# Performance work log

Measured on AMD Instinct MI355X. Metric: run time of the kernel, lower is better.

## Reference

```python
import jax, jax.numpy as jnp
import numpy as np
import math

DIM = 2048
N_HEADS = 16
HEAD_DIM = 128
BATCH = 2
T = 2048
EPS = 1e-5


def setup_inputs() -> dict:
    key = jax.random.key(0)
    ks = jax.random.split(key, 16)
    s = lambda fan_in: 1.0 / math.sqrt(fan_in)
    d = {}
    d['x'] = jax.random.normal(ks[0], (BATCH, T, DIM), dtype=jnp.float32)
    d['start_pos'] = 0
    # attention projections (weights stored [in, out])
    d['wq'] = jax.random.uniform(ks[1], (DIM, N_HEADS * HEAD_DIM), minval=-s(DIM), maxval=s(DIM))
    d['bq'] = jnp.zeros((N_HEADS * HEAD_DIM,), jnp.float32)
    d['wk'] = jax.random.uniform(ks[2], (DIM, HEAD_DIM), minval=-s(DIM), maxval=s(DIM))
    d['bk'] = jnp.zeros((HEAD_DIM,), jnp.float32)
    d['wv'] = jax.random.uniform(ks[3], (DIM, HEAD_DIM), minval=-s(DIM), maxval=s(DIM))
    d['bv'] = jnp.zeros((HEAD_DIM,), jnp.float32)
    d['wo'] = jax.random.uniform(ks[4], (N_HEADS * HEAD_DIM, DIM), minval=-s(N_HEADS * HEAD_DIM), maxval=s(N_HEADS * HEAD_DIM))
    d['bo'] = jnp.zeros((DIM,), jnp.float32)
    # layernorms
    d['ln1_g'] = jnp.ones((DIM,), jnp.float32)
    d['ln1_b'] = jnp.zeros((DIM,), jnp.float32)
    d['ln2_g'] = jnp.ones((DIM,), jnp.float32)
    d['ln2_b'] = jnp.zeros((DIM,), jnp.float32)
    # MLP (dim -> 4*dim -> dim), dropout p=0 is a no-op
    d['w1'] = jax.random.uniform(ks[5], (DIM, 4 * DIM), minval=-s(DIM), maxval=s(DIM))
    d['b1'] = jnp.zeros((4 * DIM,), jnp.float32)
    d['w2'] = jax.random.uniform(ks[6], (4 * DIM, DIM), minval=-s(4 * DIM), maxval=s(4 * DIM))
    d['b2'] = jnp.zeros((DIM,), jnp.float32)
    return d


def _layernorm(h, g, b):
    mu = jnp.mean(h, axis=-1, keepdims=True)
    var = jnp.mean(jnp.square(h - mu), axis=-1, keepdims=True)
    return (h - mu) * jax.lax.rsqrt(var + EPS) * g + b


def reference(x, start_pos, wq, bq, wk, bk, wv, bv, wo, bo, ln1_g, ln1_b, ln2_g, ln2_b, w1, b1, w2, b2):
    B, Tq, D = x.shape
    hd = wk.shape[1]
    H = wq.shape[1] // hd
    # --- MQA attention on pre-LN input (prefill: no kv cache) ---
    h = _layernorm(x, ln1_g, ln1_b)
    q = (h @ wq + bq).reshape(B, Tq, H, hd)          # [B,T,H,hd]
    k = h @ wk + bk                                   # [B,T,hd] single shared head
    v = h @ wv + bv                                   # [B,T,hd]
    scores = jnp.einsum('bthc,bsc->bhts', q, k) / math.sqrt(hd)
    causal = jnp.where(jnp.tril(jnp.ones((Tq, Tq), dtype=bool)), 0.0, -jnp.inf).astype(scores.dtype)
    attn = jax.nn.softmax(scores + causal, axis=-1)   # [B,H,T,T]
    ctx = jnp.einsum('bhts,bsc->bthc', attn, v).reshape(B, Tq, H * hd)
    out = ctx @ wo + bo
    x = x + out
    # --- GELU MLP (exact erf gelu, torch default) ---
    h2 = _layernorm(x, ln2_g, ln2_b)
    x = x + jax.nn.gelu(h2 @ w1 + b1, approximate=False) @ w2 + b2
    k_cat = k[:, None]                                # [B,1,T,hd]
    v_cat = v[:, None]
    return (x, k_cat, v_cat)
```

## Files before the change

### kernel.cpp

```cpp
#include <hip/hip_runtime.h>
#include <stdint.h>

#define DIMSZ 2048
#define HD 128
#define NH 16
#define BATCH 2
#define SEQ 2048
#define MROWS (BATCH*SEQ)
#define FFDIM (4*DIMSZ)
#define NQKV (DIMSZ + 2*HD)

typedef float f32x4 __attribute__((ext_vector_type(4)));
typedef __bf16 bf16x8 __attribute__((ext_vector_type(8)));
typedef __bf16 bf16_t;

__device__ __forceinline__ void async16(const void* g, void* l) {
  __builtin_amdgcn_global_load_lds(
      (const __attribute__((address_space(1))) void*)(uintptr_t)g,
      (__attribute__((address_space(3))) void*)(uint32_t)(uintptr_t)l,
      16, 0, 0);
}

__device__ __forceinline__ float gelu_f(float x) {
  return 0.5f * x * (1.0f + erff(x * 0.70710678118654752f));
}

__device__ __forceinline__ void hard_barrier() {
  asm volatile("" ::: "memory");
  __builtin_amdgcn_s_barrier();
  asm volatile("" ::: "memory");
}

__global__ __launch_bounds__(256)
void k_transpose_f32_bf16(const float* __restrict__ src, bf16_t* __restrict__ dst,
                          int R, int C) {
  __shared__ float tile[32][33];
  int c0 = blockIdx.x * 32, r0 = blockIdx.y * 32;
  int tx = threadIdx.x & 31, ty = threadIdx.x >> 5;
#pragma unroll
  for (int i = 0; i < 32; i += 8)
    tile[ty + i][tx] = src[(size_t)(r0 + ty + i) * C + (c0 + tx)];
  __syncthreads();
#pragma unroll
  for (int i = 0; i < 32; i += 8)
    dst[(size_t)(c0 + ty + i) * R + (r0 + tx)] = (bf16_t)tile[tx][ty + i];
}

__global__ __launch_bounds__(256)
void k_transpose_v(const bf16_t* __restrict__ v, bf16_t* __restrict__ vt) {
  __shared__ bf16_t tile[32][33];
  int b = blockIdx.z;
  int t0 = blockIdx.x * 32, d0 = blockIdx.y * 32;
  int tx = threadIdx.x & 31, ty = threadIdx.x >> 5;
#pragma unroll
  for (int i = 0; i < 32; i += 8)
    tile[ty + i][tx] = v[((size_t)(b * SEQ + t0 + ty + i)) * HD + d0 + tx];
  __syncthreads();
#pragma unroll
  for (int i = 0; i < 32; i += 8)
    vt[((size_t)(b * HD + d0 + ty + i)) * SEQ + t0 + tx] = tile[tx][ty + i];
}

__global__ __launch_bounds__(256)
void k_layernorm(const float* __restrict__ x, const float* __restrict__ g,
                 const float* __restrict__ bb, bf16_t* __restrict__ out) {
  int row = blockIdx.x;
  const float* xr = x + (size_t)row * DIMSZ;
  int t = threadIdx.x;
  float vals[8];
  float s = 0.f, s2 = 0.f;
#pragma unroll
  for (int i = 0; i < 8; ++i) {
    float v = xr[t + i * 256];
    vals[i] = v; s += v; s2 += v * v;
  }
#pragma unroll
  for (int o = 1; o < 64; o <<= 1) { s += __shfl_xor(s, o); s2 += __shfl_xor(s2, o); }
  __shared__ float red[8];
  if ((t & 63) == 0) { red[t >> 6] = s; red[4 + (t >> 6)] = s2; }
  __syncthreads();
  s = red[0] + red[1] + red[2] + red[3];
  s2 = red[4] + red[5] + red[6] + red[7];
  float mu = s * (1.0f / DIMSZ);
  float rstd = rsqrtf(s2 * (1.0f / DIMSZ) - mu * mu + 1e-5f);
  bf16_t* orow = out + (size_t)row * DIMSZ;
#pragma unroll
  for (int i = 0; i < 8; ++i) {
    int c = t + i * 256;
    orow[c] = (bf16_t)((vals[i] - mu) * rstd * g[c] + bb[c]);
  }
}

template <int FN>
__device__ __forceinline__ void gemm8_loop(
    const bf16_t* __restrict__ A, const bf16_t* __restrict__ BT, int K,
    int bm, int bn, f32x4 (&acc)[8][FN], bf16_t* sh) {
  constexpr int BH = FN >> 1;
  constexpr int BN = FN * 64;
  const int tid = threadIdx.x;
  const int lane = tid & 63, lr = lane & 15, lg = lane >> 4;
  const int wave = tid >> 6, wm = wave >> 2, wn = wave & 3;
  bf16_t* const Ab0 = sh;
  bf16_t* const Bb0 = sh + 32768;
  const bf16_t* const Ag = A + (size_t)bm * 256 * K;
  const bf16_t* const Bg = BT + (size_t)bn * BN * K;

  auto stage = [&](const bf16_t* gbase, bf16_t* lbase, int h, int t) {
#pragma unroll
    for (int j = 0; j < 2; ++j) {
      int flat = (tid + j * 512) * 8;
      int r = flat >> 6, kp = flat & 63;
      int ks = kp ^ ((r & 7) << 3);
      async16(gbase + (size_t)(h * 128 + r) * K + t * 64 + ks, lbase + flat);
    }
  };
  auto stA = [&](int c, int h, int t) { stage(Ag, Ab0 + (c * 2 + h) * 8192, h, t); };
  auto stB = [&](int c, int h, int t) { stage(Bg, Bb0 + (c * BH + h) * 8192, h, t); };

  const int xsw = (lr & 7) << 3;
  bf16x8 a_[8], b_[FN][2];
  auto lda = [&](int c, int kk) {
    const bf16_t* base = Ab0 + (c * 2 + wm) * 8192;
#pragma unroll
    for (int mf = 0; mf < 8; ++mf)
      a_[mf] = *(const bf16x8*)(base + (mf * 16 + lr) * 64 + ((kk + lg * 8) ^ xsw));
  };
  auto ldb = [&](int c) {
#pragma unroll
    for (int nf = 0; nf < FN; ++nf) {
      int row = wn * (FN * 16) + nf * 16 + lr;
      const bf16_t* base =
          Bb0 + (c * BH + (BH == 2 ? (row >> 7) : 0)) * 8192 + (row & 127) * 64;
#pragma unroll
      for (int kx = 0; kx < 2; ++kx)
        b_[nf][kx] = *(const bf16x8*)(base + ((kx * 32 + lg * 8) ^ xsw));
    }
  };

#define LGKM0 asm volatile("s_waitcnt lgkmcnt(0)" ::: "memory");
#define VMC_STEADY                                                   \
  if (BH == 2) { asm volatile("s_waitcnt vmcnt(6)" ::: "memory"); }  \
  else         { asm volatile("s_waitcnt vmcnt(4)" ::: "memory"); }
#define MFMA_HALF(M0, KX)                                            \
  __builtin_amdgcn_s_setprio(1);                                     \
  _Pragma("unroll")                                                  \
  for (int mf = 0; mf < 4; ++mf)                                     \
    _Pragma("unroll")                                                \
    for (int nf = 0; nf < FN; ++nf)                                  \
      acc[(M0) + mf][nf] = __builtin_amdgcn_mfma_f32_16x16x32_bf16(  \
          a_[(M0) + mf], b_[nf][KX], acc[(M0) + mf][nf], 0, 0, 0);   \
  __builtin_amdgcn_s_setprio(0);

  const int nit = K >> 7;

  stA(0, 0, 0); stA(0, 1, 0);
  stB(0, 0, 0); if (BH == 2) stB(0, 1, 0);
  stB(1, 0, 1); if (BH == 2) stB(1, 1, 1);
  stA(1, 0, 1);
  VMC_STEADY;
  hard_barrier();

  for (int i = 0; i < nit; ++i) {
    const int t1 = 2 * i + 1, t2 = 2 * i + 2, t3 = 2 * i + 3;
    const bool g2 = (i < nit - 1);
    lda(0, 0); ldb(0);
    stA(1, 1, t1);
    hard_barrier(); LGKM0;
    MFMA_HALF(0, 0)
    hard_barrier();
    if (g2) stB(0, 0, t2);
    hard_barrier();
    MFMA_HALF(4, 0)
    hard_barrier();
    lda(0, 32);
    if (g2 && BH == 2) stB(0, 1, t2);
    hard_barrier(); LGKM0;
    MFMA_HALF(0, 1)
    hard_barrier();
    if (g2) stA(0, 0, t2);
    if (i == nit - 1) { asm volatile("s_waitcnt vmcnt(0)" ::: "memory"); }
    else { VMC_STEADY; }
    hard_barrier();
    MFMA_HALF(4, 1)
    hard_barrier();
    lda(1, 0); ldb(1);
    if (g2) stA(0, 1, t2);
    hard_barrier(); LGKM0;
    MFMA_HALF(0, 0)
    hard_barrier();
    if (g2) stB(1, 0, t3);
    hard_barrier();
    MFMA_HALF(4, 0)
    hard_barrier();
    lda(1, 32);
    if (g2 && BH == 2) stB(1, 1, t3);
    hard_barrier(); LGKM0;
    MFMA_HALF(0, 1)
    hard_barrier();
    if (g2) {
      stA(1, 0, t3);
      VMC_STEADY;
    }
    hard_barrier();
    MFMA_HALF(4, 1)
    hard_barrier();
  }
#undef LGKM0
#undef VMC_STEADY
#undef MFMA_HALF
}

template <int FN, int EPI>
__global__ __launch_bounds__(512, 1)
void k_gemm8(const bf16_t* __restrict__ A, const bf16_t* __restrict__ BT,
             const float* __restrict__ bias, const float* __restrict__ res,
             float* __restrict__ outF, bf16_t* __restrict__ outB, int N, int K) {
  extern __shared__ __align__(16) bf16_t sh8[];
  constexpr int BN = FN * 64;
  int nt = N / BN;
  int bm = blockIdx.x / nt, bn = blockIdx.x % nt;
  f32x4 acc[8][FN] = {};
  gemm8_loop<FN>(A, BT, K, bm, bn, acc, sh8);
  int tid = threadIdx.x, wave = tid >> 6, lane = tid & 63, lr = lane & 15, lg = lane >> 4;
  int wm = wave >> 2, wn = wave & 3;
  int row0 = bm * 256 + wm * 128 + lg * 4;
  int col0 = bn * BN + wn * (FN * 16) + lr;
#pragma unroll
  for (int nf = 0; nf < FN; ++nf) {
    int c = col0 + nf * 16;
    float bi = bias[c];
#pragma unroll
    for (int mf = 0; mf < 8; ++mf) {
#pragma unroll
      for (int j = 0; j < 4; ++j) {
        int r = row0 + mf * 16 + j;
        size_t idx = (size_t)r * N + c;
        float v = acc[mf][nf][j] + bi;
        if (EPI & 1) v = gelu_f(v);
        if (EPI & 2) v += res[idx];
        if (EPI & 4) outF[idx] = v;
        if (EPI & 8) outB[idx] = (bf16_t)v;
      }
    }
  }
}

__global__ __launch_bounds__(512, 1)
void k_gemm8_qkv(const bf16_t* __restrict__ A, const bf16_t* __restrict__ BT,
                 const float* __restrict__ bq, const float* __restrict__ bk,
                 const float* __restrict__ bv,
                 bf16_t* __restrict__ qb, float* __restrict__ outk,
                 float* __restrict__ outv, bf16_t* __restrict__ kbf,
                 bf16_t* __restrict__ vbf, int K) {
  extern __shared__ __align__(16) bf16_t sh8[];
  const int nt = NQKV / 256;
  int bm = blockIdx.x / nt, bn = blockIdx.x % nt;
  f32x4 acc[8][4] = {};
  gemm8_loop<4>(A, BT, K, bm, bn, acc, sh8);
  int tid = threadIdx.x, wave = tid >> 6, lane = tid & 63, lr = lane & 15, lg = lane >> 4;
  int wm = wave >> 2, wn = wave & 3;
  int row0 = bm * 256 + wm * 128 + lg * 4;
  int col0 = bn * 256 + wn * 64 + lr;
#pragma unroll
  for (int nf = 0; nf < 4; ++nf) {
    int c = col0 + nf * 16;
    float bi = (c < 2048) ? bq[c] : (c < 2176 ? bk[c - 2048] : bv[c - 2176]);
#pragma unroll
    for (int mf = 0; mf < 8; ++mf) {
#pragma unroll
      for (int j = 0; j < 4; ++j) {
        int r = row0 + mf * 16 + j;
        float v = acc[mf][nf][j] + bi;
        if (c < 2048) {
          qb[(size_t)r * DIMSZ + c] = (bf16_t)v;
        } else if (c < 2176) {
          int cc = c - 2048;
          outk[(size_t)r * HD + cc] = v;
          kbf[(size_t)r * HD + cc] = (bf16_t)v;
        } else {
          int cc = c - 2176;
          outv[(size_t)r * HD + cc] = v;
          vbf[(size_t)r * HD + cc] = (bf16_t)v;
        }
      }
    }
  }
}

__global__ __launch_bounds__(256, 2)
void k_attn(const bf16_t* __restrict__ q, const bf16_t* __restrict__ k,
            const bf16_t* __restrict__ vt, bf16_t* __restrict__ ctx) {
  __shared__ __align__(16) bf16_t Ks[2][64 * 128];
  __shared__ __align__(16) bf16_t Vs[2][128 * 64];
  __shared__ bf16_t Pw[4][16][72];
  int pp = blockIdx.x, h = blockIdx.y, b = blockIdx.z;
  int tid = threadIdx.x, wave = tid >> 6, lane = tid & 63, lr = lane & 15, lg = lane >> 4;
  const bf16_t* kb = k + (size_t)b * SEQ * HD;
  const bf16_t* vb = vt + (size_t)b * HD * SEQ;

#define STAGE_TILE(buf, s0_)                                                      \
  {                                                                               \
    _Pragma("unroll")                                                             \
    for (int i = 0; i < 4; ++i) {                                                 \
      int flat = (i * 256 + tid) * 8;                                             \
      int kr = flat >> 7, kc = flat & 127;                                        \
      int ksrc = (((kc >> 3) ^ (kr & 7)) << 3) | (kc & 7);                        \
      async16(kb + (size_t)((s0_) + kr) * HD + ksrc, (void*)(Ks[buf] + flat));    \
      int vr = flat >> 6, vc = flat & 63;                                         \
      int vsrc = (((vc >> 3) ^ (vr & 7)) << 3) | (vc & 7);                        \
      async16(vb + (size_t)vr * SEQ + (s0_) + vsrc, (void*)(Vs[buf] + flat));     \
    }                                                                             \
  }

  for (int half = 0; half < 2; ++half) {
    int qt = half ? (31 - pp) : pp;
    int q0 = qt * 64;
    int qw = q0 + wave * 16;
    const bf16_t* qbase = q + ((size_t)(b * SEQ + qw + lr)) * DIMSZ + h * HD;
    bf16x8 qf[4];
#pragma unroll
    for (int kk = 0; kk < 4; ++kk) qf[kk] = *(const bf16x8*)(qbase + kk * 32 + lg * 8);
    f32x4 o[8] = {};
    float m_[4], l_[4];
#pragma unroll
    for (int j = 0; j < 4; ++j) { m_[j] = -3.0e38f; l_[j] = 0.f; }
    int qglob0 = qw + lg * 4;
    int ntiles = qt + 1;

    STAGE_TILE(0, 0)
    __syncthreads();
    for (int t = 0; t < ntiles; ++t) {
      int cur = t & 1;
      if (t + 1 < ntiles) STAGE_TILE(cur ^ 1, (t + 1) * 64)
      int s0 = t * 64;
      const bf16_t* Kc = Ks[cur];
      const bf16_t* Vc = Vs[cur];
      f32x4 sf[4] = {};
#pragma unroll
      for (int nf = 0; nf < 4; ++nf) {
        int R = nf * 16 + lr;
#pragma unroll
        for (int kk = 0; kk < 4; ++kk)
          sf[nf] = __builtin_amdgcn_mfma_f32_16x16x32_bf16(
              qf[kk],
              *(const bf16x8*)(Kc + R * 128 + (((kk * 4 + lg) ^ (R & 7)) << 3)),
              sf[nf], 0, 0, 0);
      }
#pragma unroll
      for (int nf = 0; nf < 4; ++nf) {
        int col = s0 + nf * 16 + lr;
#pragma unroll
        for (int j = 0; j < 4; ++j) {
          float v = sf[nf][j] * 0.088388347648318447f;
          sf[nf][j] = (col <= qglob0 + j) ? v : -3.0e38f;
        }
      }
      float mx[4];
#pragma unroll
      for (int j = 0; j < 4; ++j)
        mx[j] = fmaxf(fmaxf(sf[0][j], sf[1][j]), fmaxf(sf[2][j], sf[3][j]));
#pragma unroll
      for (int o_ = 1; o_ < 16; o_ <<= 1)
#pragma unroll
        for (int j = 0; j < 4; ++j) mx[j] = fmaxf(mx[j], __shfl_xor(mx[j], o_));
      float fsc[4], mn[4];
#pragma unroll
      for (int j = 0; j < 4; ++j) {
        mn[j] = fmaxf(m_[j], mx[j]);
        fsc[j] = __expf(m_[j] - mn[j]);
        m_[j] = mn[j];
      }
      float ps[4] = {0.f, 0.f, 0.f, 0.f};
#pragma unroll
      for (int nf = 0; nf < 4; ++nf)
#pragma unroll
        for (int j = 0; j < 4; ++j) {
          float pv = __expf(sf[nf][j] - mn[j]);
          ps[j] += pv;
          Pw[wave][lg * 4 + j][nf * 16 + lr] = (bf16_t)pv;
        }
#pragma unroll
      for (int o_ = 1; o_ < 16; o_ <<= 1)
#pragma unroll
        for (int j = 0; j < 4; ++j) ps[j] += __shfl_xor(ps[j], o_);
#pragma unroll
      for (int j = 0; j < 4; ++j) l_[j] = l_[j] * fsc[j] + ps[j];
#pragma unroll
      for (int df = 0; df < 8; ++df)
#pragma unroll
        for (int j = 0; j < 4; ++j) o[df][j] *= fsc[j];
      asm volatile("" ::: "memory");
      bf16x8 pa[2];
#pragma unroll
      for (int kk = 0; kk < 2; ++kk)
        pa[kk] = *(const bf16x8*)(&Pw[wave][lr][kk * 32 + lg * 8]);
#pragma unroll
      for (int df = 0; df < 8; ++df) {
        int R = df * 16 + lr;
#pragma unroll
        for (int kk = 0; kk < 2; ++kk)
          o[df] = __builtin_amdgcn_mfma_f32_16x16x32_bf16(
              pa[kk],
              *(const bf16x8*)(Vc + R * 64 + (((kk * 4 + lg) ^ (R & 7)) << 3)),
              o[df], 0, 0, 0);
      }
      __syncthreads();
    }
    bf16_t* cb = ctx + ((size_t)(b * SEQ + qw)) * DIMSZ + h * HD;
#pragma unroll
    for (int df = 0; df < 8; ++df)
#pragma unroll
      for (int j = 0; j < 4; ++j)
        cb[(size_t)(lg * 4 + j) * DIMSZ + df * 16 + lr] = (bf16_t)(o[df][j] / l_[j]);
  }
#undef STAGE_TILE
}

extern "C" void kernel_launch(void* const* d_in, const int* in_sizes, int n_in,
                              void* d_out, int out_size, void* d_ws, size_t ws_size,
                              hipStream_t stream) {
  const float* x   = (const float*)d_in[0];
  const float* wq  = (const float*)d_in[2];
  const float* bq  = (const float*)d_in[3];
  const float* wk  = (const float*)d_in[4];
  const float* bk  = (const float*)d_in[5];
  const float* wv  = (const float*)d_in[6];
  const float* bv  = (const float*)d_in[7];
  const float* wo  = (const float*)d_in[8];
  const float* bo  = (const float*)d_in[9];
  const float* g1  = (const float*)d_in[10];
  const float* be1 = (const float*)d_in[11];
  const float* g2  = (const float*)d_in[12];
  const float* be2 = (const float*)d_in[13];
  const float* w1  = (const float*)d_in[14];
  const float* bb1 = (const float*)d_in[15];
  const float* w2  = (const float*)d_in[16];
  const float* bb2 = (const float*)d_in[17];

  float* outx = (float*)d_out;
  float* outk = outx + (size_t)MROWS * DIMSZ;
  float* outv = outk + (size_t)MROWS * HD;

  char* p = (char*)d_ws;
  auto alloc = [&](size_t bytes) -> char* {
    char* r = p;
    p += (bytes + 255) & ~(size_t)255;
    return r;
  };
  bf16_t* wqkvT = (bf16_t*)alloc((size_t)NQKV * DIMSZ * 2);
  bf16_t* woT = (bf16_t*)alloc((size_t)DIMSZ * DIMSZ * 2);
  bf16_t* w1T = (bf16_t*)alloc((size_t)FFDIM * DIMSZ * 2);
  bf16_t* w2T = (bf16_t*)alloc((size_t)DIMSZ * FFDIM * 2);
  bf16_t* hb  = (bf16_t*)alloc((size_t)MROWS * DIMSZ * 2);
  bf16_t* qb  = (bf16_t*)alloc((size_t)MROWS * DIMSZ * 2);
  bf16_t* kbf = (bf16_t*)alloc((size_t)MROWS * HD * 2);
  bf16_t* vbf = (bf16_t*)alloc((size_t)MROWS * HD * 2);
  bf16_t* vtb = (bf16_t*)alloc((size_t)BATCH * HD * SEQ * 2);
  bf16_t* f1b = (bf16_t*)alloc((size_t)MROWS * FFDIM * 2);
  (void)ws_size; (void)in_sizes; (void)n_in; (void)out_size;

  dim3 blk(256);
  const int LDS4 = 131072;
  const int LDS2 = 98304;
  k_transpose_f32_bf16<<<dim3(DIMSZ / 32, DIMSZ / 32), blk, 0, stream>>>(wq, wqkvT, DIMSZ, DIMSZ);
  k_transpose_f32_bf16<<<dim3(HD / 32, DIMSZ / 32), blk, 0, stream>>>(wk, wqkvT + (size_t)2048 * DIMSZ, DIMSZ, HD);
  k_transpose_f32_bf16<<<dim3(HD / 32, DIMSZ / 32), blk, 0, stream>>>(wv, wqkvT + (size_t)2176 * DIMSZ, DIMSZ, HD);
  k_transpose_f32_bf16<<<dim3(DIMSZ / 32, DIMSZ / 32), blk, 0, stream>>>(wo, woT, DIMSZ, DIMSZ);
  k_transpose_f32_bf16<<<dim3(FFDIM / 32, DIMSZ / 32), blk, 0, stream>>>(w1, w1T, DIMSZ, FFDIM);
  k_transpose_f32_bf16<<<dim3(DIMSZ / 32, FFDIM / 32), blk, 0, stream>>>(w2, w2T, FFDIM, DIMSZ);
  k_layernorm<<<MROWS, blk, 0, stream>>>(x, g1, be1, hb);
  k_gemm8_qkv<<<(MROWS / 256) * (NQKV / 256), 512, LDS4, stream>>>(
      hb, wqkvT, bq, bk, bv, qb, outk, outv, kbf, vbf, DIMSZ);
  k_transpose_v<<<dim3(SEQ / 32, HD / 32, BATCH), blk, 0, stream>>>(vbf, vtb);
  k_attn<<<dim3(SEQ / 64 / 2, NH, BATCH), blk, 0, stream>>>(qb, kbf, vtb, hb);
  k_gemm8<2, 6><<<(MROWS / 256) * (DIMSZ / 128), 512, LDS2, stream>>>(
      hb, woT, bo, x, outx, nullptr, DIMSZ, DIMSZ);
  k_layernorm<<<MROWS, blk, 0, stream>>>(outx, g2, be2, qb);
  k_gemm8<4, 9><<<(MROWS / 256) * (FFDIM / 256), 512, LDS4, stream>>>(
      qb, w1T, bb1, nullptr, nullptr, f1b, FFDIM, DIMSZ);
  k_gemm8<2, 6><<<(MROWS / 256) * (DIMSZ / 128), 512, LDS2, stream>>>(
      f1b, w2T, bb2, outx, outx, nullptr, DIMSZ, FFDIM);
}
```

Measured before the change: 594.5 us.

## Split-K FFN2 GEMM with atomic accumulation and wider 256-column tiles

```diff
diff --git a/kernel.cpp b/kernel.cpp
--- a/kernel.cpp
+++ b/kernel.cpp
@@ -93,8 +93,8 @@
 
 template <int FN>
 __device__ __forceinline__ void gemm8_loop(
-    const bf16_t* __restrict__ A, const bf16_t* __restrict__ BT, int K,
-    int bm, int bn, f32x4 (&acc)[8][FN], bf16_t* sh) {
+    const bf16_t* __restrict__ A, const bf16_t* __restrict__ BT,
+    int ld, int Kloop, int bm, int bn, f32x4 (&acc)[8][FN], bf16_t* sh) {
   constexpr int BH = FN >> 1;
   constexpr int BN = FN * 64;
   const int tid = threadIdx.x;
@@ -102,8 +102,8 @@
   const int wave = tid >> 6, wm = wave >> 2, wn = wave & 3;
   bf16_t* const Ab0 = sh;
   bf16_t* const Bb0 = sh + 32768;
-  const bf16_t* const Ag = A + (size_t)bm * 256 * K;
-  const bf16_t* const Bg = BT + (size_t)bn * BN * K;
+  const bf16_t* const Ag = A + (size_t)bm * 256 * ld;
+  const bf16_t* const Bg = BT + (size_t)bn * BN * ld;
 
   auto stage = [&](const bf16_t* gbase, bf16_t* lbase, int h, int t) {
 #pragma unroll
@@ -111,7 +111,7 @@
       int flat = (tid + j * 512) * 8;
       int r = flat >> 6, kp = flat & 63;
       int ks = kp ^ ((r & 7) << 3);
-      async16(gbase + (size_t)(h * 128 + r) * K + t * 64 + ks, lbase + flat);
+      async16(gbase + (size_t)(h * 128 + r) * ld + t * 64 + ks, lbase + flat);
     }
   };
   auto stA = [&](int c, int h, int t) { stage(Ag, Ab0 + (c * 2 + h) * 8192, h, t); };
@@ -151,7 +151,7 @@
           a_[(M0) + mf], b_[nf][KX], acc[(M0) + mf][nf], 0, 0, 0);   \
   __builtin_amdgcn_s_setprio(0);
 
-  const int nit = K >> 7;
+  const int nit = Kloop >> 7;
 
   stA(0, 0, 0); stA(0, 1, 0);
   stB(0, 0, 0); if (BH == 2) stB(0, 1, 0);
@@ -210,53 +210,102 @@
 #undef MFMA_HALF
 }
 
-template <int FN, int EPI>
 __global__ __launch_bounds__(512, 1)
-void k_gemm8(const bf16_t* __restrict__ A, const bf16_t* __restrict__ BT,
+void k_oproj(const bf16_t* __restrict__ A, const bf16_t* __restrict__ BT,
              const float* __restrict__ bias, const float* __restrict__ res,
-             float* __restrict__ outF, bf16_t* __restrict__ outB, int N, int K) {
+             float* __restrict__ outF) {
   extern __shared__ __align__(16) bf16_t sh8[];
-  constexpr int BN = FN * 64;
-  int nt = N / BN;
+  const int nt = DIMSZ / 128;
   int bm = blockIdx.x / nt, bn = blockIdx.x % nt;
-  f32x4 acc[8][FN] = {};
-  gemm8_loop<FN>(A, BT, K, bm, bn, acc, sh8);
+  f32x4 acc[8][2] = {};
+  gemm8_loop<2>(A, BT, DIMSZ, DIMSZ, bm, bn, acc, sh8);
   int tid = threadIdx.x, wave = tid >> 6, lane = tid & 63, lr = lane & 15, lg = lane >> 4;
   int wm = wave >> 2, wn = wave & 3;
   int row0 = bm * 256 + wm * 128 + lg * 4;
-  int col0 = bn * BN + wn * (FN * 16) + lr;
-#pragma unroll
-  for (int nf = 0; nf < FN; ++nf) {
+  int col0 = bn * 128 + wn * 32 + lr;
+#pragma unroll
+  for (int nf = 0; nf < 2; ++nf) {
     int c = col0 + nf * 16;
     float bi = bias[c];
 #pragma unroll
-    for (int mf = 0; mf < 8; ++mf) {
+    for (int mf = 0; mf < 8; ++mf)
 #pragma unroll
       for (int j = 0; j < 4; ++j) {
         int r = row0 + mf * 16 + j;
-        size_t idx = (size_t)r * N + c;
-        float v = acc[mf][nf][j] + bi;
-        if (EPI & 1) v = gelu_f(v);
-        if (EPI & 2) v += res[idx];
-        if (EPI & 4) outF[idx] = v;
-        if (EPI & 8) outB[idx] = (bf16_t)v;
-      }
-    }
+        size_t idx = (size_t)r * DIMSZ + c;
+        outF[idx] = acc[mf][nf][j] + bi + res[idx];
+      }
   }
 }
 
 __global__ __launch_bounds__(512, 1)
-void k_gemm8_qkv(const bf16_t* __restrict__ A, const bf16_t* __restrict__ BT,
-                 const float* __restrict__ bq, const float* __restrict__ bk,
-                 const float* __restrict__ bv,
-                 bf16_t* __restrict__ qb, float* __restrict__ outk,
-                 float* __restrict__ outv, bf16_t* __restrict__ kbf,
-                 bf16_t* __restrict__ vbf, int K) {
+void k_ffn1(const bf16_t* __restrict__ A, const bf16_t* __restrict__ BT,
+            const float* __restrict__ bias, bf16_t* __restrict__ outB) {
+  extern __shared__ __align__(16) bf16_t sh8[];
+  const int nt = FFDIM / 256;
+  int bm = blockIdx.x / nt, bn = blockIdx.x % nt;
+  f32x4 acc[8][4] = {};
+  gemm8_loop<4>(A, BT, DIMSZ, DIMSZ, bm, bn, acc, sh8);
+  int tid = threadIdx.x, wave = tid >> 6, lane = tid & 63, lr = lane & 15, lg = lane >> 4;
+  int wm = wave >> 2, wn = wave & 3;
+  int row0 = bm * 256 + wm * 128 + lg * 4;
+  int col0 = bn * 256 + wn * 64 + lr;
+#pragma unroll
+  for (int nf = 0; nf < 4; ++nf) {
+    int c = col0 + nf * 16;
+    float bi = bias[c];
+#pragma unroll
+    for (int mf = 0; mf < 8; ++mf)
+#pragma unroll
+      for (int j = 0; j < 4; ++j) {
+        int r = row0 + mf * 16 + j;
+        outB[(size_t)r * FFDIM + c] = (bf16_t)gelu_f(acc[mf][nf][j] + bi);
+      }
+  }
+}
+
+__global__ __launch_bounds__(512, 1)
+void k_ffn2(const bf16_t* __restrict__ A, const bf16_t* __restrict__ BT,
+            const float* __restrict__ bias, float* __restrict__ outF) {
+  extern __shared__ __align__(16) bf16_t sh8[];
+  int bid = blockIdx.x;
+  int kh = bid >> 7;
+  int tile = bid & 127;
+  int bm = tile >> 3, bn = tile & 7;
+  f32x4 acc[8][4] = {};
+  gemm8_loop<4>(A + kh * (FFDIM / 2), BT + kh * (FFDIM / 2), FFDIM, FFDIM / 2,
+                bm, bn, acc, sh8);
+  int tid = threadIdx.x, wave = tid >> 6, lane = tid & 63, lr = lane & 15, lg = lane >> 4;
+  int wm = wave >> 2, wn = wave & 3;
+  int row0 = bm * 256 + wm * 128 + lg * 4;
+  int col0 = bn * 256 + wn * 64 + lr;
+#pragma unroll
+  for (int nf = 0; nf < 4; ++nf) {
+    int c = col0 + nf * 16;
+    float bi = kh ? 0.f : bias[c];
+#pragma unroll
+    for (int mf = 0; mf < 8; ++mf)
+#pragma unroll
+      for (int j = 0; j < 4; ++j) {
+        int r = row0 + mf * 16 + j;
+        __hip_atomic_fetch_add(&outF[(size_t)r * DIMSZ + c], acc[mf][nf][j] + bi,
+                               __ATOMIC_RELAXED, __HIP_MEMORY_SCOPE_AGENT);
+      }
+  }
+}
+
+__global__ __launch_bounds__(512, 1)
+void k_qkv(const bf16_t* __restrict__ A, const bf16_t* __restrict__ BT,
+           const float* __restrict__ bq, const float* __restrict__ bk,
+           const float* __restrict__ bv,
+           bf16_t* __restrict__ qb, float* __restrict__ outk,
+           float* __restrict__ outv, bf16_t* __restrict__ kbf,
+           bf16_t* __restrict__ vbf) {
   extern __shared__ __align__(16) bf16_t sh8[];
   const int nt = NQKV / 256;
   int bm = blockIdx.x / nt, bn = blockIdx.x % nt;
   f32x4 acc[8][4] = {};
-  gemm8_loop<4>(A, BT, K, bm, bn, acc, sh8);
+  gemm8_loop<4>(A, BT, DIMSZ, DIMSZ, bm, bn, acc, sh8);
   int tid = threadIdx.x, wave = tid >> 6, lane = tid & 63, lr = lane & 15, lg = lane >> 4;
   int wm = wave >> 2, wn = wave & 3;
   int row0 = bm * 256 + wm * 128 + lg * 4;
@@ -469,15 +518,12 @@
   k_transpose_f32_bf16<<<dim3(FFDIM / 32, DIMSZ / 32), blk, 0, stream>>>(w1, w1T, DIMSZ, FFDIM);
   k_transpose_f32_bf16<<<dim3(DIMSZ / 32, FFDIM / 32), blk, 0, stream>>>(w2, w2T, FFDIM, DIMSZ);
   k_layernorm<<<MROWS, blk, 0, stream>>>(x, g1, be1, hb);
-  k_gemm8_qkv<<<(MROWS / 256) * (NQKV / 256), 512, LDS4, stream>>>(
-      hb, wqkvT, bq, bk, bv, qb, outk, outv, kbf, vbf, DIMSZ);
+  k_qkv<<<(MROWS / 256) * (NQKV / 256), 512, LDS4, stream>>>(
+      hb, wqkvT, bq, bk, bv, qb, outk, outv, kbf, vbf);
   k_transpose_v<<<dim3(SEQ / 32, HD / 32, BATCH), blk, 0, stream>>>(vbf, vtb);
   k_attn<<<dim3(SEQ / 64 / 2, NH, BATCH), blk, 0, stream>>>(qb, kbf, vtb, hb);
-  k_gemm8<2, 6><<<(MROWS / 256) * (DIMSZ / 128), 512, LDS2, stream>>>(
-      hb, woT, bo, x, outx, nullptr, DIMSZ, DIMSZ);
+  k_oproj<<<(MROWS / 256) * (DIMSZ / 128), 512, LDS2, stream>>>(hb, woT, bo, x, outx);
   k_layernorm<<<MROWS, blk, 0, stream>>>(outx, g2, be2, qb);
-  k_gemm8<4, 9><<<(MROWS / 256) * (FFDIM / 256), 512, LDS4, stream>>>(
-      qb, w1T, bb1, nullptr, nullptr, f1b, FFDIM, DIMSZ);
-  k_gemm8<2, 6><<<(MROWS / 256) * (DIMSZ / 128), 512, LDS2, stream>>>(
-      f1b, w2T, bb2, outx, outx, nullptr, DIMSZ, FFDIM);
-}
+  k_ffn1<<<(MROWS / 256) * (FFDIM / 256), 512, LDS4, stream>>>(qb, w1T, bb1, f1b);
+  k_ffn2<<<256, 512, LDS4, stream>>>(f1b, w2T, bb2, outx);
+}
```

New measurement: 585.1 us. About the same (-1.6%).
